# Performance work log

Hardware: AMD Instinct MI355X
Metric: run time of the kernel (lower is better)

## Reference

```python
import jax, jax.numpy as jnp
import numpy as np
import math

B, S, D, H = 1, 4096, 512, 8


def setup_inputs() -> dict:
    key = jax.random.key(0)
    ks = jax.random.split(key, 7)
    s = 0.02
    return {
        "queries": jax.random.normal(ks[0], (B, S, D), jnp.float32),
        "keys": jax.random.normal(ks[1], (B, S, D), jnp.float32),
        "values": jax.random.normal(ks[2], (B, S, D), jnp.float32),
        "Wq": jax.random.normal(ks[3], (D, D), jnp.float32) * s,
        "Wk": jax.random.normal(ks[4], (D, D), jnp.float32) * s,
        "Wv": jax.random.normal(ks[5], (D, D), jnp.float32) * s,
        "Wo": jax.random.normal(ks[6], (D, D), jnp.float32) * s,
    }


def _split_heads(x, num_heads):
    # (B, S, D) -> (B*H, S, D/H), matching transpose_qkv
    b, s, d = x.shape
    x = x.reshape(b, s, num_heads, d // num_heads).transpose(0, 2, 1, 3)
    return x.reshape(b * num_heads, s, d // num_heads)


def _merge_heads(x, num_heads):
    # (B*H, S, dh) -> (B, S, D), matching transpose_output
    bh, s, dh = x.shape
    x = x.reshape(bh // num_heads, num_heads, s, dh).transpose(0, 2, 1, 3)
    return x.reshape(bh // num_heads, s, num_heads * dh)


def reference(queries, keys, values, Wq, Wk, Wv, Wo):
    q = _split_heads(queries @ Wq.T, H)  # (B*H, S, dh)
    k = _split_heads(keys @ Wk.T, H)
    v = _split_heads(values @ Wv.T, H)
    dh = q.shape[-1]
    scores = jnp.einsum('bqd,bkd->bqk', q, k) / math.sqrt(dh)  # (B*H, Sq, Sk)
    # NOTE: original torch code applies softmax over dim=0 (the batch*heads axis).
    attn = jax.nn.softmax(scores, axis=0)
    out = jnp.einsum('bqk,bkd->bqd', attn, v)  # dropout p=0 -> identity
    out = _merge_heads(out, H)  # (B, S, D)
    return out @ Wo.T
```

## Files before the change

### kernel.cpp

```cpp
#include <hip/hip_runtime.h>
#include <hip/hip_bf16.h>

constexpr int S_ = 4096;
constexpr int D_ = 512;

using f32x4 = __attribute__((ext_vector_type(4))) float;
using s16x4 = __attribute__((ext_vector_type(4))) short;
using s16x8 = __attribute__((ext_vector_type(8))) short;
using u16x4 = __attribute__((ext_vector_type(4))) unsigned short;
using u16x8 = __attribute__((ext_vector_type(8))) unsigned short;

__device__ __forceinline__ unsigned short f2bf(float f) {
    union { float f; unsigned u; } v; v.f = f;
    unsigned r = v.u + 0x7FFFu + ((v.u >> 16) & 1u);
    return (unsigned short)(r >> 16);
}

__device__ __forceinline__ float bf2f(unsigned short u) {
    union { unsigned u; float f; } v; v.u = (unsigned)u << 16; return v.f;
}

__device__ __forceinline__ unsigned pack_bf16(float lo, float hi) {
    float2 t; t.x = lo; t.y = hi;
    __hip_bfloat162 b = __float22bfloat162_rn(t);
    union { __hip_bfloat162 b; unsigned u; } cv; cv.b = b; return cv.u;
}

__device__ __forceinline__ f32x4 mfma16(s16x4 a, s16x4 b, f32x4 c) {
#if __has_builtin(__builtin_amdgcn_mfma_f32_16x16x16bf16_1k)
    return __builtin_amdgcn_mfma_f32_16x16x16bf16_1k(a, b, c, 0, 0, 0);
#elif __has_builtin(__builtin_amdgcn_mfma_f32_16x16x16_bf16)
    return __builtin_amdgcn_mfma_f32_16x16x16_bf16(a, b, c, 0, 0, 0);
#else
    asm volatile("v_mfma_f32_16x16x16_bf16 %0, %1, %2, %0" : "+v"(c) : "v"(a), "v"(b));
    return c;
#endif
}

template<bool IN_BF16, int OUT_MODE>
__global__ __launch_bounds__(256) void proj_kernel(const void* __restrict__ Xv,
                                                   const float* __restrict__ W,
                                                   void* __restrict__ Yv, float scale) {
    constexpr int BM = 128, BN = 64, BK = 64;
    __shared__ unsigned short Xs[BM][BK + 8];
    __shared__ unsigned short Ws_[BN][BK + 8];
    const int m0 = blockIdx.x * BM;
    const int n0 = blockIdx.y * BN;
    const int tid = threadIdx.x;
    const int lane = tid & 63, w = tid >> 6;
    const int wi = w >> 1, wj = w & 1;
    const int lr = lane & 15, lg = lane >> 4;

    f32x4 acc[4][2] = {};

    for (int kt = 0; kt < D_ / BK; ++kt) {
        const int k0 = kt * BK;
        __syncthreads();
        if (IN_BF16) {
            const unsigned short* X = (const unsigned short*)Xv;
#pragma unroll
            for (int r = 0; r < 4; ++r) {
                int idx = tid + r * 256;
                int row = idx >> 3, c8 = idx & 7;
                u16x8 vv = *(const u16x8*)(X + (size_t)(m0 + row) * D_ + k0 + c8 * 8);
                *(u16x8*)&Xs[row][c8 * 8] = vv;
            }
        } else {
            const float* X = (const float*)Xv;
#pragma unroll
            for (int r = 0; r < 8; ++r) {
                int idx = tid + r * 256;
                int row = idx >> 4, c4 = idx & 15;
                f32x4 vv = *(const f32x4*)(X + (size_t)(m0 + row) * D_ + k0 + c4 * 4);
                u16x4 o;
#pragma unroll
                for (int t = 0; t < 4; ++t) o[t] = f2bf(vv[t]);
                *(u16x4*)&Xs[row][c4 * 4] = o;
            }
        }
#pragma unroll
        for (int r = 0; r < 4; ++r) {
            int idx = tid + r * 256;
            int row = idx >> 4, c4 = idx & 15;
            f32x4 vv = *(const f32x4*)(W + (size_t)(n0 + row) * D_ + k0 + c4 * 4);
            u16x4 o;
#pragma unroll
            for (int t = 0; t < 4; ++t) o[t] = f2bf(vv[t]);
            *(u16x4*)&Ws_[row][c4 * 4] = o;
        }
        __syncthreads();
#pragma unroll
        for (int ks = 0; ks < 2; ++ks) {
            s16x8 a[4], b[2];
#pragma unroll
            for (int mf = 0; mf < 4; ++mf)
                a[mf] = *(const s16x8*)&Xs[wi * 64 + mf * 16 + lr][ks * 32 + lg * 8];
#pragma unroll
            for (int nf = 0; nf < 2; ++nf)
                b[nf] = *(const s16x8*)&Ws_[wj * 32 + nf * 16 + lr][ks * 32 + lg * 8];
#pragma unroll
            for (int mf = 0; mf < 4; ++mf)
#pragma unroll
                for (int nf = 0; nf < 2; ++nf)
                    acc[mf][nf] = __builtin_amdgcn_mfma_f32_16x16x32_bf16(a[mf], b[nf], acc[mf][nf], 0, 0, 0);
        }
    }

    if (OUT_MODE == 1) {
        __syncthreads();
        unsigned short* T = &Xs[0][0] + w * 2304;
#pragma unroll
        for (int mf = 0; mf < 4; ++mf)
#pragma unroll
            for (int nf = 0; nf < 2; ++nf)
#pragma unroll
                for (int r = 0; r < 4; ++r) {
                    int n_loc = nf * 16 + lr;
                    int i_loc = mf * 16 + lg * 4 + r;
                    T[n_loc * 72 + i_loc] = f2bf(acc[mf][nf][r] * scale);
                }
        __syncthreads();
        unsigned short* Y = (unsigned short*)Yv;
#pragma unroll
        for (int rr = 0; rr < 4; ++rr) {
            int chunk = lane + rr * 64;
            int n_loc = chunk >> 3, c8 = chunk & 7;
            u16x8 vv = *(const u16x8*)&T[n_loc * 72 + c8 * 8];
            *(u16x8*)(Y + (size_t)(n0 + wj * 32 + n_loc) * S_ + m0 + wi * 64 + c8 * 8) = vv;
        }
    } else {
#pragma unroll
        for (int mf = 0; mf < 4; ++mf)
#pragma unroll
            for (int nf = 0; nf < 2; ++nf)
#pragma unroll
                for (int r = 0; r < 4; ++r) {
                    int i = m0 + wi * 64 + mf * 16 + lg * 4 + r;
                    int n = n0 + wj * 32 + nf * 16 + lr;
                    float val = acc[mf][nf][r] * scale;
                    if (OUT_MODE == 0) ((unsigned short*)Yv)[(size_t)i * D_ + n] = f2bf(val);
                    else                ((float*)Yv)[(size_t)i * D_ + n] = val;
                }
    }
}

__global__ __launch_bounds__(256, 2) void attn_kernel(const unsigned short* __restrict__ Qp,
                                                      const unsigned short* __restrict__ Kp,
                                                      const unsigned short* __restrict__ VpT,
                                                      unsigned short* __restrict__ partial,
                                                      int tpc) {
    __shared__ float den[2][4][2][64][4];
    const int nblk = gridDim.x;
    const int cpx = nblk >> 3;
    const int bid = blockIdx.x;
    const int rank = (bid & 7) * cpx + (bid >> 3);
    const int jc = rank >> 7;
    const int i0 = (rank & 127) * 32;
    const int tid = threadIdx.x;
    const int lane = tid & 63, w = tid >> 6;
    const int lr = lane & 15, lg = lane >> 4;
    const int kb = w * 128;

    s16x8 q[2][4];
#pragma unroll
    for (int f = 0; f < 2; ++f)
#pragma unroll
        for (int kf = 0; kf < 4; ++kf)
            q[f][kf] = *(const s16x8*)(Qp + (size_t)(i0 + f * 16 + lr) * D_ + kb + kf * 32 + lg * 8);

    f32x4 acc[8][2] = {};

    const int t0 = jc * tpc;
    const int t1 = t0 + tpc;

    for (int t = t0; t < t1; ++t) {
        const int j0 = t * 16;
        const int slot = t & 1;

        s16x8 kA[4];
#pragma unroll
        for (int kf = 0; kf < 4; ++kf)
            kA[kf] = *(const s16x8*)(Kp + (size_t)(j0 + lr) * D_ + kb + kf * 32 + lg * 8);
        s16x4 vA[8];
#pragma unroll
        for (int df = 0; df < 8; ++df)
            vA[df] = *(const s16x4*)(VpT + (size_t)(kb + df * 16 + lr) * S_ + j0 + lg * 4);

        f32x4 sf[2][2] = {};
        __builtin_amdgcn_s_setprio(1);
#pragma unroll
        for (int hh = 0; hh < 2; ++hh)
#pragma unroll
            for (int ks = 0; ks < 2; ++ks)
#pragma unroll
                for (int f = 0; f < 2; ++f)
                    sf[hh][f] = __builtin_amdgcn_mfma_f32_16x16x32_bf16(kA[hh * 2 + ks], q[f][hh * 2 + ks], sf[hh][f], 0, 0, 0);
        __builtin_amdgcn_s_setprio(0);

#pragma unroll
        for (int hh = 0; hh < 2; ++hh)
#pragma unroll
            for (int f = 0; f < 2; ++f)
#pragma unroll
                for (int r = 0; r < 4; ++r)
                    sf[hh][f][r] = exp2f(sf[hh][f][r]);
#pragma unroll
        for (int f = 0; f < 2; ++f)
            *(f32x4*)den[slot][w][f][lane] = sf[0][f] + sf[1][f];

        asm volatile("s_waitcnt lgkmcnt(0)\n\ts_barrier" ::: "memory");

        f32x4 dt[2];
#pragma unroll
        for (int f = 0; f < 2; ++f) {
            dt[f] = *(const f32x4*)den[slot][0][f][lane];
#pragma unroll
            for (int wp = 1; wp < 4; ++wp)
                dt[f] += *(const f32x4*)den[slot][wp][f][lane];
        }

        s16x4 pb[2][2];
#pragma unroll
        for (int f = 0; f < 2; ++f) {
            f32x4 rd;
#pragma unroll
            for (int r = 0; r < 4; ++r) rd[r] = __builtin_amdgcn_rcpf(dt[f][r]);
#pragma unroll
            for (int hh = 0; hh < 2; ++hh) {
                union { s16x4 v; uint2 u; } pc;
                pc.u.x = pack_bf16(sf[hh][f][0] * rd[0], sf[hh][f][1] * rd[1]);
                pc.u.y = pack_bf16(sf[hh][f][2] * rd[2], sf[hh][f][3] * rd[3]);
                pb[hh][f] = pc.v;
            }
        }

        __builtin_amdgcn_s_setprio(1);
#pragma unroll
        for (int df = 0; df < 8; ++df)
#pragma unroll
            for (int f = 0; f < 2; ++f)
                acc[df][f] = mfma16(vA[df], pb[df >> 2][f], acc[df][f]);
        __builtin_amdgcn_s_setprio(0);
    }

    unsigned short* P = partial + (size_t)jc * S_ * D_;
#pragma unroll
    for (int df = 0; df < 8; ++df)
#pragma unroll
        for (int f = 0; f < 2; ++f) {
            union { u16x4 v; uint2 u; } pc;
            pc.u.x = pack_bf16(acc[df][f][0], acc[df][f][1]);
            pc.u.y = pack_bf16(acc[df][f][2], acc[df][f][3]);
            *(u16x4*)(P + (size_t)(i0 + f * 16 + lr) * D_ + kb + df * 16 + lg * 4) = pc.v;
        }
}

__global__ __launch_bounds__(256) void reduceN_kernel(const unsigned short* __restrict__ partial,
                                                      unsigned short* __restrict__ outp, int njc) {
    size_t base = ((size_t)blockIdx.x * 256 + threadIdx.x) * 8;
    float s[8] = {};
    for (int c = 0; c < njc; ++c) {
        u16x8 vv = *(const u16x8*)(partial + (size_t)c * S_ * D_ + base);
#pragma unroll
        for (int e = 0; e < 8; ++e) s[e] += bf2f(vv[e]);
    }
    u16x8 o;
#pragma unroll
    for (int e = 0; e < 8; ++e) o[e] = f2bf(s[e]);
    *(u16x8*)(outp + base) = o;
}

extern "C" void kernel_launch(void* const* d_in, const int* in_sizes, int n_in,
                              void* d_out, int out_size, void* d_ws, size_t ws_size,
                              hipStream_t stream) {
    const float* q  = (const float*)d_in[0];
    const float* k  = (const float*)d_in[1];
    const float* v  = (const float*)d_in[2];
    const float* Wq = (const float*)d_in[3];
    const float* Wk = (const float*)d_in[4];
    const float* Wv = (const float*)d_in[5];
    const float* Wo = (const float*)d_in[6];

    int njc = 2;
    if      (ws_size >= ((size_t)(16 + 4 * 8) << 20)) njc = 8;
    else if (ws_size >= ((size_t)(16 + 4 * 4) << 20)) njc = 4;

    char* ws = (char*)d_ws;
    unsigned short* Qp  = (unsigned short*)(ws);
    unsigned short* Kp  = (unsigned short*)(ws + (4u  << 20));
    unsigned short* VpT = (unsigned short*)(ws + (8u  << 20));
    unsigned short* part= (unsigned short*)(ws + (12u << 20));
    unsigned short* ao  = (unsigned short*)(ws + ((size_t)(12 + 4 * njc) << 20));

    const float qscale = 0.125f * 1.44269504088896340736f;

    dim3 pb(256);
    dim3 pg(S_ / 128, D_ / 64);
    proj_kernel<false, 0><<<pg, pb, 0, stream>>>(q, Wq, Qp, qscale);
    proj_kernel<false, 0><<<pg, pb, 0, stream>>>(k, Wk, Kp, 1.0f);
    proj_kernel<false, 1><<<pg, pb, 0, stream>>>(v, Wv, VpT, 1.0f);
    attn_kernel<<<dim3(128 * njc), pb, 0, stream>>>(Qp, Kp, VpT, part, S_ / 16 / njc);
    reduceN_kernel<<<dim3(S_ * D_ / 2048), pb, 0, stream>>>(part, ao, njc);
    proj_kernel<true, 2><<<pg, pb, 0, stream>>>(ao, Wo, (float*)d_out, 1.0f);
}
```

Before: 244.1 us.

## Split attention across eight waves per head and prefetch K tiles

```diff
diff --git a/kernel.cpp b/kernel.cpp
--- a/kernel.cpp
+++ b/kernel.cpp
@@ -26,15 +26,13 @@
     union { __hip_bfloat162 b; unsigned u; } cv; cv.b = b; return cv.u;
 }
 
+__device__ __forceinline__ float fexp2(float x) {
+    return exp2f(x);
+}
+
 __device__ __forceinline__ f32x4 mfma16(s16x4 a, s16x4 b, f32x4 c) {
-#if __has_builtin(__builtin_amdgcn_mfma_f32_16x16x16bf16_1k)
-    return __builtin_amdgcn_mfma_f32_16x16x16bf16_1k(a, b, c, 0, 0, 0);
-#elif __has_builtin(__builtin_amdgcn_mfma_f32_16x16x16_bf16)
-    return __builtin_amdgcn_mfma_f32_16x16x16_bf16(a, b, c, 0, 0, 0);
-#else
     asm volatile("v_mfma_f32_16x16x16_bf16 %0, %1, %2, %0" : "+v"(c) : "v"(a), "v"(b));
     return c;
-#endif
 }
 
 template<bool IN_BF16, int OUT_MODE>
@@ -144,12 +142,12 @@
     }
 }
 
-__global__ __launch_bounds__(256, 2) void attn_kernel(const unsigned short* __restrict__ Qp,
+__global__ __launch_bounds__(512, 4) void attn_kernel(const unsigned short* __restrict__ Qp,
                                                       const unsigned short* __restrict__ Kp,
                                                       const unsigned short* __restrict__ VpT,
                                                       unsigned short* __restrict__ partial,
                                                       int tpc) {
-    __shared__ float den[2][4][2][64][4];
+    __shared__ float den[2][8][2][64][4];
     const int nblk = gridDim.x;
     const int cpx = nblk >> 3;
     const int bid = blockIdx.x;
@@ -159,93 +157,106 @@
     const int tid = threadIdx.x;
     const int lane = tid & 63, w = tid >> 6;
     const int lr = lane & 15, lg = lane >> 4;
-    const int kb = w * 128;
-
-    s16x8 q[2][4];
+    const int kb = w * 64;
+
+    const int koff = lr * D_ + kb + lg * 8;
+    int voff[4];
+#pragma unroll
+    for (int df = 0; df < 4; ++df)
+        voff[df] = (kb + df * 16 + lr) * S_ + lg * 4;
+
+    s16x8 q[2][2];
 #pragma unroll
     for (int f = 0; f < 2; ++f)
 #pragma unroll
-        for (int kf = 0; kf < 4; ++kf)
+        for (int kf = 0; kf < 2; ++kf)
             q[f][kf] = *(const s16x8*)(Qp + (size_t)(i0 + f * 16 + lr) * D_ + kb + kf * 32 + lg * 8);
 
-    f32x4 acc[8][2] = {};
+    f32x4 acc[4][2] = {};
 
     const int t0 = jc * tpc;
     const int t1 = t0 + tpc;
 
-    for (int t = t0; t < t1; ++t) {
+    s16x8 kA[2], kB[2];
+    {
+        const unsigned short* kbase = Kp + (size_t)t0 * 16 * D_;
+        kA[0] = *(const s16x8*)(kbase + koff);
+        kA[1] = *(const s16x8*)(kbase + koff + 32);
+    }
+
+    auto step = [&](int t, int slot, s16x8 (&kc)[2], s16x8 (&kn)[2]) {
         const int j0 = t * 16;
-        const int slot = t & 1;
-
-        s16x8 kA[4];
-#pragma unroll
-        for (int kf = 0; kf < 4; ++kf)
-            kA[kf] = *(const s16x8*)(Kp + (size_t)(j0 + lr) * D_ + kb + kf * 32 + lg * 8);
-        s16x4 vA[8];
-#pragma unroll
-        for (int df = 0; df < 8; ++df)
-            vA[df] = *(const s16x4*)(VpT + (size_t)(kb + df * 16 + lr) * S_ + j0 + lg * 4);
-
-        f32x4 sf[2][2] = {};
+        const unsigned short* vb = VpT + j0;
+        s16x4 vA[4];
+#pragma unroll
+        for (int df = 0; df < 4; ++df)
+            vA[df] = *(const s16x4*)(vb + voff[df]);
+        __builtin_amdgcn_sched_barrier(0);
+        const unsigned short* kbase = Kp + (size_t)(j0 + 16) * D_;
+        kn[0] = *(const s16x8*)(kbase + koff);
+        kn[1] = *(const s16x8*)(kbase + koff + 32);
+        __builtin_amdgcn_sched_barrier(0);
+
+        f32x4 sf[2];
         __builtin_amdgcn_s_setprio(1);
 #pragma unroll
-        for (int hh = 0; hh < 2; ++hh)
-#pragma unroll
-            for (int ks = 0; ks < 2; ++ks)
-#pragma unroll
-                for (int f = 0; f < 2; ++f)
-                    sf[hh][f] = __builtin_amdgcn_mfma_f32_16x16x32_bf16(kA[hh * 2 + ks], q[f][hh * 2 + ks], sf[hh][f], 0, 0, 0);
+        for (int f = 0; f < 2; ++f) {
+            f32x4 s = {0.f, 0.f, 0.f, 0.f};
+            s = __builtin_amdgcn_mfma_f32_16x16x32_bf16(kc[0], q[f][0], s, 0, 0, 0);
+            s = __builtin_amdgcn_mfma_f32_16x16x32_bf16(kc[1], q[f][1], s, 0, 0, 0);
+            sf[f] = s;
+        }
         __builtin_amdgcn_s_setprio(0);
 
 #pragma unroll
-        for (int hh = 0; hh < 2; ++hh)
+        for (int f = 0; f < 2; ++f) {
+#pragma unroll
+            for (int r = 0; r < 4; ++r)
+                sf[f][r] = fexp2(sf[f][r]);
+            *(f32x4*)den[slot][w][f][lane] = sf[f];
+        }
+
+        asm volatile("s_waitcnt lgkmcnt(0)" ::: "memory");
+        __builtin_amdgcn_s_barrier();
+
+        f32x4 dt[2];
+#pragma unroll
+        for (int f = 0; f < 2; ++f) {
+            dt[f] = *(const f32x4*)den[slot][0][f][lane];
+#pragma unroll
+            for (int wp = 1; wp < 8; ++wp)
+                dt[f] += *(const f32x4*)den[slot][wp][f][lane];
+        }
+
+        s16x4 pb[2];
+#pragma unroll
+        for (int f = 0; f < 2; ++f) {
+            f32x4 rd;
+#pragma unroll
+            for (int r = 0; r < 4; ++r) rd[r] = __builtin_amdgcn_rcpf(dt[f][r]);
+            union { s16x4 v; uint2 u; } pc;
+            pc.u.x = pack_bf16(sf[f][0] * rd[0], sf[f][1] * rd[1]);
+            pc.u.y = pack_bf16(sf[f][2] * rd[2], sf[f][3] * rd[3]);
+            pb[f] = pc.v;
+        }
+
+        __builtin_amdgcn_s_setprio(1);
+#pragma unroll
+        for (int df = 0; df < 4; ++df)
 #pragma unroll
             for (int f = 0; f < 2; ++f)
-#pragma unroll
-                for (int r = 0; r < 4; ++r)
-                    sf[hh][f][r] = exp2f(sf[hh][f][r]);
-#pragma unroll
-        for (int f = 0; f < 2; ++f)
-            *(f32x4*)den[slot][w][f][lane] = sf[0][f] + sf[1][f];
-
-        asm volatile("s_waitcnt lgkmcnt(0)\n\ts_barrier" ::: "memory");
-
-        f32x4 dt[2];
-#pragma unroll
-        for (int f = 0; f < 2; ++f) {
-            dt[f] = *(const f32x4*)den[slot][0][f][lane];
-#pragma unroll
-            for (int wp = 1; wp < 4; ++wp)
-                dt[f] += *(const f32x4*)den[slot][wp][f][lane];
-        }
-
-        s16x4 pb[2][2];
-#pragma unroll
-        for (int f = 0; f < 2; ++f) {
-            f32x4 rd;
-#pragma unroll
-            for (int r = 0; r < 4; ++r) rd[r] = __builtin_amdgcn_rcpf(dt[f][r]);
-#pragma unroll
-            for (int hh = 0; hh < 2; ++hh) {
-                union { s16x4 v; uint2 u; } pc;
-                pc.u.x = pack_bf16(sf[hh][f][0] * rd[0], sf[hh][f][1] * rd[1]);
-                pc.u.y = pack_bf16(sf[hh][f][2] * rd[2], sf[hh][f][3] * rd[3]);
-                pb[hh][f] = pc.v;
-            }
-        }
-
-        __builtin_amdgcn_s_setprio(1);
-#pragma unroll
-        for (int df = 0; df < 8; ++df)
-#pragma unroll
-            for (int f = 0; f < 2; ++f)
-                acc[df][f] = mfma16(vA[df], pb[df >> 2][f], acc[df][f]);
+                acc[df][f] = mfma16(vA[df], pb[f], acc[df][f]);
         __builtin_amdgcn_s_setprio(0);
+    };
+
+    for (int tt = t0; tt < t1; tt += 2) {
+        step(tt,     0, kA, kB);
+        step(tt + 1, 1, kB, kA);
     }
 
     unsigned short* P = partial + (size_t)jc * S_ * D_;
 #pragma unroll
-    for (int df = 0; df < 8; ++df)
+    for (int df = 0; df < 4; ++df)
 #pragma unroll
         for (int f = 0; f < 2; ++f) {
             union { u16x4 v; uint2 u; } pc;
@@ -299,7 +310,7 @@
     proj_kernel<false, 0><<<pg, pb, 0, stream>>>(q, Wq, Qp, qscale);
     proj_kernel<false, 0><<<pg, pb, 0, stream>>>(k, Wk, Kp, 1.0f);
     proj_kernel<false, 1><<<pg, pb, 0, stream>>>(v, Wv, VpT, 1.0f);
-    attn_kernel<<<dim3(128 * njc), pb, 0, stream>>>(Qp, Kp, VpT, part, S_ / 16 / njc);
+    attn_kernel<<<dim3(128 * njc), dim3(512), 0, stream>>>(Qp, Kp, VpT, part, S_ / 16 / njc);
     reduceN_kernel<<<dim3(S_ * D_ / 2048), pb, 0, stream>>>(part, ao, njc);
     proj_kernel<true, 2><<<pg, pb, 0, stream>>>(ao, Wo, (float*)d_out, 1.0f);
 }
```

Result: no change. 241.0 us (-1.3%).

## Retile attention to 16 query rows by 64 key rows per iteration

Applied to the files above, without the earlier changes.

```diff
diff --git a/kernel.cpp b/kernel.cpp
--- a/kernel.cpp
+++ b/kernel.cpp
@@ -27,14 +27,8 @@
 }
 
 __device__ __forceinline__ f32x4 mfma16(s16x4 a, s16x4 b, f32x4 c) {
-#if __has_builtin(__builtin_amdgcn_mfma_f32_16x16x16bf16_1k)
-    return __builtin_amdgcn_mfma_f32_16x16x16bf16_1k(a, b, c, 0, 0, 0);
-#elif __has_builtin(__builtin_amdgcn_mfma_f32_16x16x16_bf16)
-    return __builtin_amdgcn_mfma_f32_16x16x16_bf16(a, b, c, 0, 0, 0);
-#else
     asm volatile("v_mfma_f32_16x16x16_bf16 %0, %1, %2, %0" : "+v"(c) : "v"(a), "v"(b));
     return c;
-#endif
 }
 
 template<bool IN_BF16, int OUT_MODE>
@@ -148,110 +142,126 @@
                                                       const unsigned short* __restrict__ Kp,
                                                       const unsigned short* __restrict__ VpT,
                                                       unsigned short* __restrict__ partial,
-                                                      int tpc) {
-    __shared__ float den[2][4][2][64][4];
+                                                      int njc) {
+    __shared__ f32x4 den[2][4][4][64];
     const int nblk = gridDim.x;
-    const int cpx = nblk >> 3;
     const int bid = blockIdx.x;
-    const int rank = (bid & 7) * cpx + (bid >> 3);
-    const int jc = rank >> 7;
-    const int i0 = (rank & 127) * 32;
+    const int rank = (bid & 7) * (nblk >> 3) + (bid >> 3);
+    const int jc = rank >> 8;
+    const int i0 = (rank & 255) * 16;
     const int tid = threadIdx.x;
     const int lane = tid & 63, w = tid >> 6;
     const int lr = lane & 15, lg = lane >> 4;
     const int kb = w * 128;
 
-    s16x8 q[2][4];
-#pragma unroll
-    for (int f = 0; f < 2; ++f)
-#pragma unroll
-        for (int kf = 0; kf < 4; ++kf)
-            q[f][kf] = *(const s16x8*)(Qp + (size_t)(i0 + f * 16 + lr) * D_ + kb + kf * 32 + lg * 8);
-
-    f32x4 acc[8][2] = {};
-
-    const int t0 = jc * tpc;
-    const int t1 = t0 + tpc;
-
-    for (int t = t0; t < t1; ++t) {
-        const int j0 = t * 16;
+    s16x8 q[4];
+#pragma unroll
+    for (int kf = 0; kf < 4; ++kf)
+        q[kf] = *(const s16x8*)(Qp + (size_t)(i0 + lr) * D_ + kb + kf * 32 + lg * 8);
+
+    f32x4 acc[2][4] = {};
+
+    const int iters = S_ / 64 / njc;
+    const int jbase = jc * (S_ / njc);
+
+    for (int t = 0; t < iters; ++t) {
+        const int j0 = jbase + t * 64;
         const int slot = t & 1;
 
-        s16x8 kA[4];
-#pragma unroll
-        for (int kf = 0; kf < 4; ++kf)
-            kA[kf] = *(const s16x8*)(Kp + (size_t)(j0 + lr) * D_ + kb + kf * 32 + lg * 8);
-        s16x4 vA[8];
-#pragma unroll
-        for (int df = 0; df < 8; ++df)
-            vA[df] = *(const s16x4*)(VpT + (size_t)(kb + df * 16 + lr) * S_ + j0 + lg * 4);
-
-        f32x4 sf[2][2] = {};
+        s16x8 kA[4][4];
+#pragma unroll
+        for (int jf = 0; jf < 4; ++jf)
+#pragma unroll
+            for (int kf = 0; kf < 4; ++kf)
+                kA[jf][kf] = *(const s16x8*)(Kp + (size_t)(j0 + jf * 16 + lr) * D_ + kb + kf * 32 + lg * 8);
+
+        s16x4 va[8], vb[8];
+#pragma unroll
+        for (int hh = 0; hh < 2; ++hh)
+#pragma unroll
+            for (int df = 0; df < 4; ++df)
+                va[hh * 4 + df] = *(const s16x4*)(VpT + (size_t)(kb + hh * 64 + df * 16 + lr) * S_ + j0 + lg * 4);
+
+        f32x4 sf[2][4];
         __builtin_amdgcn_s_setprio(1);
 #pragma unroll
         for (int hh = 0; hh < 2; ++hh)
 #pragma unroll
-            for (int ks = 0; ks < 2; ++ks)
-#pragma unroll
-                for (int f = 0; f < 2; ++f)
-                    sf[hh][f] = __builtin_amdgcn_mfma_f32_16x16x32_bf16(kA[hh * 2 + ks], q[f][hh * 2 + ks], sf[hh][f], 0, 0, 0);
+            for (int jf = 0; jf < 4; ++jf) {
+                f32x4 s = {0.f, 0.f, 0.f, 0.f};
+                s = __builtin_amdgcn_mfma_f32_16x16x32_bf16(kA[jf][hh * 2 + 0], q[hh * 2 + 0], s, 0, 0, 0);
+                s = __builtin_amdgcn_mfma_f32_16x16x32_bf16(kA[jf][hh * 2 + 1], q[hh * 2 + 1], s, 0, 0, 0);
+                sf[hh][jf] = s;
+            }
         __builtin_amdgcn_s_setprio(0);
 
 #pragma unroll
         for (int hh = 0; hh < 2; ++hh)
 #pragma unroll
-            for (int f = 0; f < 2; ++f)
+            for (int jf = 0; jf < 4; ++jf)
 #pragma unroll
                 for (int r = 0; r < 4; ++r)
-                    sf[hh][f][r] = exp2f(sf[hh][f][r]);
-#pragma unroll
-        for (int f = 0; f < 2; ++f)
-            *(f32x4*)den[slot][w][f][lane] = sf[0][f] + sf[1][f];
-
-        asm volatile("s_waitcnt lgkmcnt(0)\n\ts_barrier" ::: "memory");
-
-        f32x4 dt[2];
-#pragma unroll
-        for (int f = 0; f < 2; ++f) {
-            dt[f] = *(const f32x4*)den[slot][0][f][lane];
+                    sf[hh][jf][r] = exp2f(sf[hh][jf][r]);
+#pragma unroll
+        for (int jf = 0; jf < 4; ++jf)
+            den[slot][w][jf][lane] = sf[0][jf] + sf[1][jf];
+
+        asm volatile("s_waitcnt lgkmcnt(0)" ::: "memory");
+        __builtin_amdgcn_s_barrier();
+
+        f32x4 dt[4];
+#pragma unroll
+        for (int jf = 0; jf < 4; ++jf) {
+            dt[jf] = den[slot][0][jf][lane];
 #pragma unroll
             for (int wp = 1; wp < 4; ++wp)
-                dt[f] += *(const f32x4*)den[slot][wp][f][lane];
-        }
-
-        s16x4 pb[2][2];
-#pragma unroll
-        for (int f = 0; f < 2; ++f) {
-            f32x4 rd;
-#pragma unroll
-            for (int r = 0; r < 4; ++r) rd[r] = __builtin_amdgcn_rcpf(dt[f][r]);
-#pragma unroll
-            for (int hh = 0; hh < 2; ++hh) {
+                dt[jf] += den[slot][wp][jf][lane];
+#pragma unroll
+            for (int r = 0; r < 4; ++r)
+                dt[jf][r] = __builtin_amdgcn_rcpf(dt[jf][r]);
+        }
+
+        s16x4 pb[2][4];
+#pragma unroll
+        for (int hh = 0; hh < 2; ++hh)
+#pragma unroll
+            for (int jf = 0; jf < 4; ++jf) {
                 union { s16x4 v; uint2 u; } pc;
-                pc.u.x = pack_bf16(sf[hh][f][0] * rd[0], sf[hh][f][1] * rd[1]);
-                pc.u.y = pack_bf16(sf[hh][f][2] * rd[2], sf[hh][f][3] * rd[3]);
-                pb[hh][f] = pc.v;
-            }
-        }
+                pc.u.x = pack_bf16(sf[hh][jf][0] * dt[jf][0], sf[hh][jf][1] * dt[jf][1]);
+                pc.u.y = pack_bf16(sf[hh][jf][2] * dt[jf][2], sf[hh][jf][3] * dt[jf][3]);
+                pb[hh][jf] = pc.v;
+            }
 
         __builtin_amdgcn_s_setprio(1);
 #pragma unroll
-        for (int df = 0; df < 8; ++df)
-#pragma unroll
-            for (int f = 0; f < 2; ++f)
-                acc[df][f] = mfma16(vA[df], pb[df >> 2][f], acc[df][f]);
+        for (int jf = 0; jf < 4; ++jf) {
+            s16x4* cur = (jf & 1) ? vb : va;
+            s16x4* nxt = (jf & 1) ? va : vb;
+            if (jf < 3) {
+#pragma unroll
+                for (int hh = 0; hh < 2; ++hh)
+#pragma unroll
+                    for (int df = 0; df < 4; ++df)
+                        nxt[hh * 4 + df] = *(const s16x4*)(VpT + (size_t)(kb + hh * 64 + df * 16 + lr) * S_ + j0 + (jf + 1) * 16 + lg * 4);
+            }
+#pragma unroll
+            for (int hh = 0; hh < 2; ++hh)
+#pragma unroll
+                for (int df = 0; df < 4; ++df)
+                    acc[hh][df] = mfma16(cur[hh * 4 + df], pb[hh][jf], acc[hh][df]);
+        }
         __builtin_amdgcn_s_setprio(0);
     }
 
     unsigned short* P = partial + (size_t)jc * S_ * D_;
 #pragma unroll
-    for (int df = 0; df < 8; ++df)
-#pragma unroll
-        for (int f = 0; f < 2; ++f) {
+    for (int hh = 0; hh < 2; ++hh)
+#pragma unroll
+        for (int df = 0; df < 4; ++df) {
             union { u16x4 v; uint2 u; } pc;
-            pc.u.x = pack_bf16(acc[df][f][0], acc[df][f][1]);
-            pc.u.y = pack_bf16(acc[df][f][2], acc[df][f][3]);
-            *(u16x4*)(P + (size_t)(i0 + f * 16 + lr) * D_ + kb + df * 16 + lg * 4) = pc.v;
+            pc.u.x = pack_bf16(acc[hh][df][0], acc[hh][df][1]);
+            pc.u.y = pack_bf16(acc[hh][df][2], acc[hh][df][3]);
+            *(u16x4*)(P + (size_t)(i0 + lr) * D_ + kb + hh * 64 + df * 16 + lg * 4) = pc.v;
         }
 }
 
@@ -299,7 +309,7 @@
     proj_kernel<false, 0><<<pg, pb, 0, stream>>>(q, Wq, Qp, qscale);
     proj_kernel<false, 0><<<pg, pb, 0, stream>>>(k, Wk, Kp, 1.0f);
     proj_kernel<false, 1><<<pg, pb, 0, stream>>>(v, Wv, VpT, 1.0f);
-    attn_kernel<<<dim3(128 * njc), pb, 0, stream>>>(Qp, Kp, VpT, part, S_ / 16 / njc);
+    attn_kernel<<<dim3(256 * njc), pb, 0, stream>>>(Qp, Kp, VpT, part, njc);
     reduceN_kernel<<<dim3(S_ * D_ / 2048), pb, 0, stream>>>(part, ao, njc);
     proj_kernel<true, 2><<<pg, pb, 0, stream>>>(ao, Wo, (float*)d_out, 1.0f);
 }
```

Result: slower. 404.4 us (+65.7%).
